# Optimization experiments

Hardware: AMD Instinct MI355X
Metric: run time of the kernel (lower is better)

Reference implementation:

```python
import jax, jax.numpy as jnp
import numpy as np

HIDDEN = 1024
HEADS = 16
HEAD_DIM = 64
B, S = 2, 2048
SCALE = 1.0 / np.sqrt(HEAD_DIM)
NEG = -1e9


def setup_inputs() -> dict:
    key = jax.random.key(0)
    k1, k2, k3, k4, k5 = jax.random.split(key, 5)
    hidden_states = jax.random.normal(k1, (B, S, HIDDEN), dtype=jnp.float32)
    # causal additive mask, broadcast over heads: [B, 1, S, S]
    causal = jnp.where(jnp.tril(jnp.ones((S, S), dtype=bool)), 0.0, NEG).astype(jnp.float32)
    attention_mask = jnp.broadcast_to(causal[None, None], (B, 1, S, S))
    std = 1.0 / np.sqrt(HIDDEN)
    Wq = jax.random.normal(k2, (HIDDEN, HEADS * HEAD_DIM), dtype=jnp.float32) * std
    Wk = jax.random.normal(k3, (HIDDEN, HEADS * HEAD_DIM), dtype=jnp.float32) * std
    Wv = jax.random.normal(k4, (HIDDEN, HEADS * HEAD_DIM), dtype=jnp.float32) * std
    Wo = jax.random.normal(k5, (HEADS * HEAD_DIM, HIDDEN), dtype=jnp.float32) * std
    return {"hidden_states": hidden_states, "attention_mask": attention_mask,
            "Wq": Wq, "Wk": Wk, "Wv": Wv, "Wo": Wo}


def reference(hidden_states, attention_mask, Wq, Wk, Wv, Wo):
    b, s, _ = hidden_states.shape
    # projections (eval mode: dropouts are identity)
    q = (hidden_states @ Wq).reshape(b, s, HEADS, HEAD_DIM).transpose(0, 2, 1, 3)  # [B,H,S,D]
    k = (hidden_states @ Wk).reshape(b, s, HEADS, HEAD_DIM).transpose(0, 2, 1, 3)
    v = (hidden_states @ Wv).reshape(b, s, HEADS, HEAD_DIM).transpose(0, 2, 1, 3)
    scores = jnp.einsum('bhqd,bhkd->bhqk', q, k) * SCALE + attention_mask  # [B,H,S,S]
    probs = jax.nn.softmax(scores, axis=-1)
    out = jnp.einsum('bhqk,bhkd->bhqd', probs, v)  # [B,H,S,D]
    out = out.transpose(0, 2, 1, 3).reshape(b, s, HEADS * HEAD_DIM)
    return out @ Wo  # [B,S,HIDDEN]
```

## Files before the change

kernel.cpp:

```cpp
#include <hip/hip_runtime.h>

typedef unsigned short u16;
typedef unsigned int u32;
typedef __bf16 bf16x8 __attribute__((ext_vector_type(8)));
typedef float f32x4 __attribute__((ext_vector_type(4)));

#define MFMA(a, b, c) __builtin_amdgcn_mfma_f32_16x16x32_bf16(a, b, c, 0, 0, 0)

#define GLD16(gsrc, ldst)                                                          \
  __builtin_amdgcn_global_load_lds(                                                \
      (const __attribute__((address_space(1))) void*)(gsrc),                       \
      (__attribute__((address_space(3))) void*)(ldst), 16, 0, 0)

#if __has_builtin(__builtin_amdgcn_exp2f)
#define EXP2(x) __builtin_amdgcn_exp2f(x)
#else
#define EXP2(x) exp2f(x)
#endif

__device__ __forceinline__ u16 f2bf(float f) {
  return __builtin_bit_cast(u16, (__bf16)f);
}

__device__ __forceinline__ u32 pk2(float a, float b) {
  __bf16 x = (__bf16)a, y = (__bf16)b;
  return (u32)__builtin_bit_cast(u16, x) | ((u32)__builtin_bit_cast(u16, y) << 16);
}

__device__ __forceinline__ float bf2f(u16 u) {
  return __builtin_bit_cast(float, ((u32)u) << 16);
}

__global__ __launch_bounds__(256) void k_cvt_x(const float* __restrict__ x,
                                               u16* __restrict__ xb) {
  int i = blockIdx.x * 256 + threadIdx.x;
  const float4* p = (const float4*)x + (size_t)i * 2;
  float4 a = p[0], b = p[1];
  uint4 o;
  o.x = pk2(a.x, a.y);
  o.y = pk2(a.z, a.w);
  o.z = pk2(b.x, b.y);
  o.w = pk2(b.z, b.w);
  *(uint4*)(xb + (size_t)i * 8) = o;
}

__global__ __launch_bounds__(256) void k_transpose_w(
    const float* __restrict__ Wq, const float* __restrict__ Wk,
    const float* __restrict__ Wv, const float* __restrict__ Wo,
    u16* __restrict__ Wt, u16* __restrict__ Wot) {
  __shared__ u16 t[32][33];
  const int k0 = blockIdx.x * 32, n0 = blockIdx.y * 32;
  const int x = threadIdx.x & 31, y = threadIdx.x >> 5;
  const float* src = (n0 < 1024) ? Wq : (n0 < 2048) ? Wk : (n0 < 3072) ? Wv : Wo;
  const int ncol = n0 & 1023;
#pragma unroll
  for (int rr = 0; rr < 4; ++rr) {
    int kl = y + rr * 8;
    t[x][kl] = f2bf(src[(size_t)(k0 + kl) * 1024 + ncol + x]);
  }
  __syncthreads();
  u16* dst = (n0 < 3072) ? (Wt + (size_t)n0 * 1024) : (Wot + (size_t)(n0 - 3072) * 1024);
#pragma unroll
  for (int rr = 0; rr < 4; ++rr) {
    int nl = y + rr * 8;
    dst[(size_t)nl * 1024 + k0 + x] = t[nl][x];
  }
}


__global__ __launch_bounds__(256) void k_gemm_qkv(const u16* __restrict__ A_,
                                                  const u16* __restrict__ Bt,
                                                  u16* __restrict__ Q,
                                                  u16* __restrict__ K,
                                                  u16* __restrict__ Vt) {
  __shared__ __align__(16) u16 As[2][128 * 32];
  __shared__ __align__(16) u16 Bs[2][128 * 32];
  const int tid = threadIdx.x;
  const int w = tid >> 6, l = tid & 63;
  const int lr = l & 15, lg = l >> 4;
  const int lin = blockIdx.y * 24 + blockIdx.x;
  const int swz = (lin & 7) * 96 + (lin >> 3);
  const int tM = (swz / 24) * 128, tN = (swz % 24) * 128;
  const int wr = w >> 1, wc = w & 1;
  const int bufsel = tN >> 10;

  const int srow = l >> 2;
  const int scol = (((l & 3) ^ ((l >> 3) & 3)) << 3);
  const u16* Ag = A_ + (size_t)(tM + srow) * 1024 + scol;
  const u16* Bg = Bt + (size_t)(tN + srow) * 1024 + scol;
  const int rs = (lr >> 1) & 3;

#define STAGE_QKV(buf, kk)                                                   \
  {                                                                          \
    GLD16(Ag + (size_t)(w * 16) * 1024 + (kk), &As[buf][(w * 16) * 32]);     \
    GLD16(Ag + (size_t)(64 + w * 16) * 1024 + (kk), &As[buf][(64 + w * 16) * 32]); \
    GLD16(Bg + (size_t)(w * 16) * 1024 + (kk), &Bs[buf][(w * 16) * 32]);     \
    GLD16(Bg + (size_t)(64 + w * 16) * 1024 + (kk), &Bs[buf][(64 + w * 16) * 32]); \
  }

  f32x4 acc[4][4] = {};
  STAGE_QKV(0, 0)
  __syncthreads();
  int cur = 0;

  if (bufsel < 2) {
    for (int t = 0; t < 32; ++t) {
      if (t < 31) STAGE_QKV(cur ^ 1, (t + 1) * 32)
      const u16* Ac = &As[cur][0];
      const u16* Bc = &Bs[cur][0];
      bf16x8 a[4], b[4];
#pragma unroll
      for (int m = 0; m < 4; ++m)
        a[m] = *(const bf16x8*)(Ac + (wr * 64 + m * 16 + lr) * 32 + ((lg ^ rs) << 3));
#pragma unroll
      for (int n = 0; n < 4; ++n)
        b[n] = *(const bf16x8*)(Bc + (wc * 64 + n * 16 + lr) * 32 + ((lg ^ rs) << 3));
#pragma unroll
      for (int m = 0; m < 4; ++m)
#pragma unroll
        for (int n = 0; n < 4; ++n) acc[m][n] = MFMA(b[n], a[m], acc[m][n]);
      __syncthreads();
      cur ^= 1;
    }
    u16* dst = bufsel ? K : Q;
    const float sc = bufsel ? 1.0f : 0.180336880111124f;
#pragma unroll
    for (int m = 0; m < 4; ++m) {
      int s = tM + wr * 64 + m * 16 + lr;
      int b_ = s >> 11, sr2 = s & 2047;
#pragma unroll
      for (int n = 0; n < 4; ++n) {
        int c = tN + wc * 64 + n * 16 + lg * 4;
        int c2 = c & 1023;
        int h = c2 >> 6, d = c2 & 63;
        uint2 val;
        val.x = pk2(acc[m][n][0] * sc, acc[m][n][1] * sc);
        val.y = pk2(acc[m][n][2] * sc, acc[m][n][3] * sc);
        *(uint2*)(dst + ((size_t)(b_ * 16 + h) * 2048 + sr2) * 64 + d) = val;
      }
    }
  } else {
    for (int t = 0; t < 32; ++t) {
      if (t < 31) STAGE_QKV(cur ^ 1, (t + 1) * 32)
      const u16* Ac = &As[cur][0];
      const u16* Bc = &Bs[cur][0];
      bf16x8 a[4], b[4];
#pragma unroll
      for (int m = 0; m < 4; ++m)
        a[m] = *(const bf16x8*)(Ac + (wr * 64 + m * 16 + lr) * 32 + ((lg ^ rs) << 3));
#pragma unroll
      for (int n = 0; n < 4; ++n)
        b[n] = *(const bf16x8*)(Bc + (wc * 64 + n * 16 + lr) * 32 + ((lg ^ rs) << 3));
#pragma unroll
      for (int m = 0; m < 4; ++m)
#pragma unroll
        for (int n = 0; n < 4; ++n) acc[m][n] = MFMA(a[m], b[n], acc[m][n]);
      __syncthreads();
      cur ^= 1;
    }
#pragma unroll
    for (int m = 0; m < 4; ++m) {
      int r0 = tM + wr * 64 + m * 16 + lg * 4;
      int b_ = r0 >> 11, s0 = r0 & 2047;
#pragma unroll
      for (int n = 0; n < 4; ++n) {
        int c = tN + wc * 64 + n * 16 + lr;
        int c2 = c & 1023;
        int h = c2 >> 6, d = c2 & 63;
        uint2 val;
        val.x = pk2(acc[m][n][0], acc[m][n][1]);
        val.y = pk2(acc[m][n][2], acc[m][n][3]);
        *(uint2*)(Vt + ((size_t)(b_ * 16 + h) * 64 + d) * 2048 + s0) = val;
      }
    }
  }
#undef STAGE_QKV
}

__global__ __launch_bounds__(256, 4) void k_attn(const u16* __restrict__ Q,
                                                 const u16* __restrict__ Kg,
                                                 const u16* __restrict__ Vtg,
                                                 u16* __restrict__ AO,
                                                 u16* __restrict__ PO,
                                                 float* __restrict__ ML) {
  __shared__ __align__(16) u16 Ks[2][64 * 64];
  __shared__ __align__(16) u16 Vs[2][64 * 64];
  __shared__ __align__(16) u16 Ps[4][16 * 64];
  const int tid = threadIdx.x;
  const int w = tid >> 6, l = tid & 63;
  const int lr = l & 15, lg = l >> 4;

  const int idx = blockIdx.x;
  const int bh = idx & 31;
  const int g = idx >> 5;
  int qt, c0;
  if (g < 16) { qt = 16 + g; c0 = 0; }
  else if (g < 32) { qt = 31 - (g - 16); c0 = 1; }
  else { qt = 15 - (g - 32); c0 = 0; }
  const int nkt = (qt < 16) ? (qt + 1) : (c0 == 0 ? 16 : qt - 15);
  const bool hasdiag = (qt < 16) || (c0 == 1);
  const int q0 = qt * 64;

  const u16* Qp = Q + (size_t)bh * 2048 * 64;
  const u16* Kp = Kg + (size_t)bh * 2048 * 64;
  const u16* Vp = Vtg + (size_t)bh * 64 * 2048;

  const int qrow = q0 + w * 16 + lr;
  bf16x8 qa0 = *(const bf16x8*)(Qp + (size_t)qrow * 64 + lg * 8);
  bf16x8 qa1 = *(const bf16x8*)(Qp + (size_t)qrow * 64 + 32 + lg * 8);

  f32x4 oacc[4] = {};
  float m_run = -1e30f, l_run = 0.f;

  const int srow = l >> 3;
  const int scol = ((l & 7) ^ srow) * 8;
  const int sw = (lr & 7) << 3;

  const u16* kptr = Kp + ((size_t)c0 * 1024 + srow) * 64 + scol;
  const u16* vptr = Vp + (size_t)srow * 2048 + c0 * 1024 + scol;

#pragma unroll
  for (int j = 0; j < 2; ++j) {
    int base = j * 32 + w * 8;
    GLD16(kptr + base * 64, &Ks[0][base * 64]);
    GLD16(vptr + (size_t)base * 2048, &Vs[0][base * 64]);
  }
  kptr += 4096;
  vptr += 64;
  __syncthreads();

  int cur = 0;

#define ATTN_TILE(DOPRE, DOMASK)                                                   \
  {                                                                                \
    if (DOPRE) {                                                                   \
      _Pragma("unroll") for (int j = 0; j < 2; ++j) {                              \
        int base = j * 32 + w * 8;                                                 \
        GLD16(kptr + base * 64, &Ks[cur ^ 1][base * 64]);                          \
        GLD16(vptr + (size_t)base * 2048, &Vs[cur ^ 1][base * 64]);                \
      }                                                                            \
      kptr += 4096;                                                                \
      vptr += 64;                                                                  \
    }                                                                              \
    f32x4 st[4];                                                                   \
    _Pragma("unroll") for (int n = 0; n < 4; ++n) {                                \
      const u16* kr = &Ks[cur][(n * 16 + lr) * 64];                                \
      bf16x8 kb0 = *(const bf16x8*)(kr + ((lg << 3) ^ sw));                        \
      bf16x8 kb1 = *(const bf16x8*)(kr + (((4 + lg) << 3) ^ sw));                  \
      f32x4 z = {0.f, 0.f, 0.f, 0.f};                                              \
      z = MFMA(kb0, qa0, z);                                                       \
      z = MFMA(kb1, qa1, z);                                                       \
      st[n] = z;                                                                   \
    }                                                                              \
    float mx = -1e30f;                                                             \
    _Pragma("unroll") for (int n = 0; n < 4; ++n)                                  \
        _Pragma("unroll") for (int j = 0; j < 4; ++j) {                            \
      float s = st[n][j];                                                          \
      if (DOMASK && (n * 16 + lg * 4 + j) > (w * 16 + lr)) s = -1e30f;             \
      st[n][j] = s;                                                                \
      mx = fmaxf(mx, s);                                                           \
    }                                                                              \
    mx = fmaxf(mx, __shfl_xor(mx, 16, 64));                                        \
    mx = fmaxf(mx, __shfl_xor(mx, 32, 64));                                        \
    const bool grow = __any(mx > m_run);                                           \
    float mnew = grow ? fmaxf(m_run, mx) : m_run;                                  \
    float rsum = 0.f;                                                              \
    _Pragma("unroll") for (int n = 0; n < 4; ++n)                                  \
        _Pragma("unroll") for (int j = 0; j < 4; ++j) {                            \
      float p = EXP2(st[n][j] - mnew);                                             \
      st[n][j] = p;                                                                \
      rsum += p;                                                                   \
    }                                                                              \
    rsum += __shfl_xor(rsum, 16, 64);                                              \
    rsum += __shfl_xor(rsum, 32, 64);                                              \
    if (grow) {                                                                    \
      float fsc = EXP2(m_run - mnew);                                              \
      l_run = l_run * fsc + rsum;                                                  \
      m_run = mnew;                                                                \
      _Pragma("unroll") for (int n = 0; n < 4; ++n)                                \
          _Pragma("unroll") for (int j = 0; j < 4; ++j) oacc[n][j] *= fsc;         \
    } else {                                                                       \
      l_run += rsum;                                                               \
    }                                                                              \
    u16* pb = &Ps[w][0];                                                           \
    _Pragma("unroll") for (int n = 0; n < 4; ++n) {                                \
      int slot = n * 2 + (lg >> 1);                                                \
      int off = lr * 64 + ((slot ^ (lr & 7)) << 3) + (lg & 1) * 4;                 \
      uint2 val;                                                                   \
      val.x = pk2(st[n][0], st[n][1]);                                             \
      val.y = pk2(st[n][2], st[n][3]);                                             \
      *(uint2*)(pb + off) = val;                                                   \
    }                                                                              \
    bf16x8 pa0 = *(const bf16x8*)(pb + lr * 64 + ((lg << 3) ^ sw));                \
    bf16x8 pa1 = *(const bf16x8*)(pb + lr * 64 + (((4 + lg) << 3) ^ sw));          \
    _Pragma("unroll") for (int n = 0; n < 4; ++n) {                                \
      const u16* vr = &Vs[cur][(n * 16 + lr) * 64];                                \
      bf16x8 vb0 = *(const bf16x8*)(vr + ((lg << 3) ^ sw));                        \
      bf16x8 vb1 = *(const bf16x8*)(vr + (((4 + lg) << 3) ^ sw));                  \
      oacc[n] = MFMA(vb0, pa0, oacc[n]);                                           \
      oacc[n] = MFMA(vb1, pa1, oacc[n]);                                           \
    }                                                                              \
  }

  for (int it = 0; it < nkt - 1; ++it) {
    ATTN_TILE(true, false);
    __syncthreads();
    cur ^= 1;
  }
  if (hasdiag) {
    ATTN_TILE(false, true);
  } else {
    ATTN_TILE(false, false);
  }
#undef ATTN_TILE

  if (qt < 16) {
    const int b_ = bh >> 4, h = bh & 15;
    const float linv = 1.0f / l_run;
    const int s = q0 + w * 16 + lr;
    u16* dst = AO + ((size_t)(b_ * 2048 + s)) * 1024 + h * 64 + lg * 4;
#pragma unroll
    for (int n = 0; n < 4; ++n) {
      uint2 val;
      val.x = pk2(oacc[n][0] * linv, oacc[n][1] * linv);
      val.y = pk2(oacc[n][2] * linv, oacc[n][3] * linv);
      *(uint2*)(dst + n * 16) = val;
    }
  } else {
    const int p = (bh * 16 + (qt - 16)) * 2 + c0;
    u16* po = PO + (size_t)p * 4096 + (size_t)(w * 16 + lr) * 64 + lg * 4;
#pragma unroll
    for (int n = 0; n < 4; ++n) {
      uint2 val;
      val.x = pk2(oacc[n][0], oacc[n][1]);
      val.y = pk2(oacc[n][2], oacc[n][3]);
      *(uint2*)(po + n * 16) = val;
    }
    if (lg == 0) {
      ML[(size_t)p * 128 + (w * 16 + lr)] = m_run;
      ML[(size_t)p * 128 + 64 + (w * 16 + lr)] = l_run;
    }
  }
}

__global__ __launch_bounds__(256) void k_combine(const u16* __restrict__ PO,
                                                 const float* __restrict__ ML,
                                                 u16* __restrict__ AO) {
  const int blk = blockIdx.x;
  const int bh = blk >> 4, qt = 16 + (blk & 15);
  const int row = threadIdx.x >> 2;
  const int dseg = (threadIdx.x & 3) * 16;
  const size_t p0 = (size_t)blk * 2;
  const float m0 = ML[p0 * 128 + row], l0 = ML[p0 * 128 + 64 + row];
  const float m1 = ML[p0 * 128 + 128 + row], l1 = ML[p0 * 128 + 192 + row];
  const float M = fmaxf(m0, m1);
  float w0 = EXP2(m0 - M), w1 = EXP2(m1 - M);
  const float inv = 1.0f / (l0 * w0 + l1 * w1);
  w0 *= inv;
  w1 *= inv;
  const u16* o0 = PO + p0 * 4096 + (size_t)row * 64 + dseg;
  const u16* o1 = o0 + 4096;
  const int b_ = bh >> 4, h = bh & 15;
  u16* dst = AO + ((size_t)(b_ * 2048 + qt * 64 + row)) * 1024 + h * 64 + dseg;
#pragma unroll
  for (int half = 0; half < 2; ++half) {
    uint4 a = *(const uint4*)(o0 + half * 8);
    uint4 b = *(const uint4*)(o1 + half * 8);
    u32 aw[4] = {a.x, a.y, a.z, a.w};
    u32 bw[4] = {b.x, b.y, b.z, b.w};
    uint4 o;
    u32 ow[4];
#pragma unroll
    for (int i = 0; i < 4; ++i) {
      float r0 = bf2f((u16)(aw[i] & 0xffffu)) * w0 + bf2f((u16)(bw[i] & 0xffffu)) * w1;
      float r1 = bf2f((u16)(aw[i] >> 16)) * w0 + bf2f((u16)(bw[i] >> 16)) * w1;
      ow[i] = pk2(r0, r1);
    }
    o.x = ow[0]; o.y = ow[1]; o.z = ow[2]; o.w = ow[3];
    *(uint4*)(dst + half * 8) = o;
  }
}

__global__ __launch_bounds__(256) void k_gemm_out(const u16* __restrict__ A_,
                                                  const u16* __restrict__ Bt,
                                                  float* __restrict__ out) {
  __shared__ __align__(16) u16 As[2][128 * 32];
  __shared__ __align__(16) u16 Bs[2][64 * 32];
  const int tid = threadIdx.x;
  const int w = tid >> 6, l = tid & 63;
  const int lr = l & 15, lg = l >> 4;
  const int lin = blockIdx.y * 16 + blockIdx.x;
  const int swz = (lin & 7) * 64 + (lin >> 3);
  const int tM = (swz / 16) * 128, tN = (swz % 16) * 64;

  const int srow = l >> 2;
  const int scol = (((l & 3) ^ ((l >> 3) & 3)) << 3);
  const u16* Ag = A_ + (size_t)(tM + srow) * 1024 + scol;
  const u16* Bg = Bt + (size_t)(tN + srow) * 1024 + scol;
  const int rs = (lr >> 1) & 3;

#define STAGE_OUT(buf, kk)                                                   \
  {                                                                          \
    GLD16(Ag + (size_t)(w * 16) * 1024 + (kk), &As[buf][(w * 16) * 32]);     \
    GLD16(Ag + (size_t)(64 + w * 16) * 1024 + (kk), &As[buf][(64 + w * 16) * 32]); \
    GLD16(Bg + (size_t)(w * 16) * 1024 + (kk), &Bs[buf][(w * 16) * 32]);     \
  }

  f32x4 acc[2][4] = {};
  STAGE_OUT(0, 0)
  __syncthreads();
  int cur = 0;
  for (int t = 0; t < 32; ++t) {
    if (t < 31) STAGE_OUT(cur ^ 1, (t + 1) * 32)
    const u16* Ac = &As[cur][0];
    const u16* Bc = &Bs[cur][0];
    bf16x8 a[2], b[4];
#pragma unroll
    for (int m = 0; m < 2; ++m)
      a[m] = *(const bf16x8*)(Ac + (w * 32 + m * 16 + lr) * 32 + ((lg ^ rs) << 3));
#pragma unroll
    for (int n = 0; n < 4; ++n)
      b[n] = *(const bf16x8*)(Bc + (n * 16 + lr) * 32 + ((lg ^ rs) << 3));
#pragma unroll
    for (int m = 0; m < 2; ++m)
#pragma unroll
      for (int n = 0; n < 4; ++n) acc[m][n] = MFMA(b[n], a[m], acc[m][n]);
    __syncthreads();
    cur ^= 1;
  }
#undef STAGE_OUT

#pragma unroll
  for (int m = 0; m < 2; ++m) {
    int s = tM + w * 32 + m * 16 + lr;
#pragma unroll
    for (int n = 0; n < 4; ++n) {
      int c = tN + n * 16 + lg * 4;
      float4 v;
      v.x = acc[m][n][0];
      v.y = acc[m][n][1];
      v.z = acc[m][n][2];
      v.w = acc[m][n][3];
      *(float4*)(out + (size_t)s * 1024 + c) = v;
    }
  }
}

extern "C" void kernel_launch(void* const* d_in, const int* in_sizes, int n_in,
                              void* d_out, int out_size, void* d_ws, size_t ws_size,
                              hipStream_t stream) {
  const float* X = (const float*)d_in[0];
  const float* Wq = (const float*)d_in[2];
  const float* Wk = (const float*)d_in[3];
  const float* Wv = (const float*)d_in[4];
  const float* Wo = (const float*)d_in[5];
  float* out = (float*)d_out;

  char* ws = (char*)d_ws;
  if (ws_size < (size_t)48 * 1024 * 1024) return;
  u16* Xb  = (u16*)(ws);
  u16* Wt  = (u16*)(ws + 8388608);
  u16* Wot = (u16*)(ws + 14680064);
  u16* Q   = (u16*)(ws + 16777216);
  u16* K   = (u16*)(ws + 25165824);
  u16* Vt  = (u16*)(ws + 33554432);
  u16* AO  = (u16*)(ws + 41943040);
  u16*   PO = (u16*)(ws);
  float* ML = (float*)(ws + 8388608);

  k_cvt_x<<<2048, 256, 0, stream>>>(X, Xb);
  k_transpose_w<<<dim3(32, 128), 256, 0, stream>>>(Wq, Wk, Wv, Wo, Wt, Wot);
  k_gemm_qkv<<<dim3(24, 32), 256, 0, stream>>>(Xb, Wt, Q, K, Vt);
  k_attn<<<1536, 256, 0, stream>>>(Q, K, Vt, AO, PO, ML);
  k_combine<<<512, 256, 0, stream>>>(PO, ML, AO);
  k_gemm_out<<<dim3(16, 32), 256, 0, stream>>>(AO, Wot, out);
}
```

Baseline: 120.2 us.

## Fuse split-KV combine into output GEMM, merge prep kernels, add MFMA priority

Merges the x-conversion and weight-transpose kernels into a single prep launch. Folds the split-KV partial combine into the output projection GEMM's A-tile staging for the second half of each sequence, which removes one kernel launch and the AO round-trip for those rows. Also raises wave priority around the MFMA sections in attention and relaxes the online-softmax rescale threshold so the running max is updated only when it grows by more than 8. The combine path replaces async global-to-LDS loads with register loads plus exp math inside the GEMM loop, which could stall it. The relaxed threshold lets un-rescaled exponentials reach up to 2^8, a small numeric risk.

```diff
diff --git a/kernel.cpp b/kernel.cpp
--- a/kernel.cpp
+++ b/kernel.cpp
@@ -31,25 +31,27 @@
   return __builtin_bit_cast(float, ((u32)u) << 16);
 }
 
-__global__ __launch_bounds__(256) void k_cvt_x(const float* __restrict__ x,
-                                               u16* __restrict__ xb) {
-  int i = blockIdx.x * 256 + threadIdx.x;
-  const float4* p = (const float4*)x + (size_t)i * 2;
-  float4 a = p[0], b = p[1];
-  uint4 o;
-  o.x = pk2(a.x, a.y);
-  o.y = pk2(a.z, a.w);
-  o.z = pk2(b.x, b.y);
-  o.w = pk2(b.z, b.w);
-  *(uint4*)(xb + (size_t)i * 8) = o;
-}
-
-__global__ __launch_bounds__(256) void k_transpose_w(
-    const float* __restrict__ Wq, const float* __restrict__ Wk,
-    const float* __restrict__ Wv, const float* __restrict__ Wo,
+__global__ __launch_bounds__(256) void k_prep(
+    const float* __restrict__ X, const float* __restrict__ Wq,
+    const float* __restrict__ Wk, const float* __restrict__ Wv,
+    const float* __restrict__ Wo, u16* __restrict__ Xb,
     u16* __restrict__ Wt, u16* __restrict__ Wot) {
   __shared__ u16 t[32][33];
-  const int k0 = blockIdx.x * 32, n0 = blockIdx.y * 32;
+  int bid = blockIdx.x;
+  if (bid < 2048) {
+    int i = bid * 256 + threadIdx.x;
+    const float4* p = (const float4*)X + (size_t)i * 2;
+    float4 a = p[0], b = p[1];
+    uint4 o;
+    o.x = pk2(a.x, a.y);
+    o.y = pk2(a.z, a.w);
+    o.z = pk2(b.x, b.y);
+    o.w = pk2(b.z, b.w);
+    *(uint4*)(Xb + (size_t)i * 8) = o;
+    return;
+  }
+  bid -= 2048;
+  const int k0 = (bid & 31) * 32, n0 = (bid >> 5) * 32;
   const int x = threadIdx.x & 31, y = threadIdx.x >> 5;
   const float* src = (n0 < 1024) ? Wq : (n0 < 2048) ? Wk : (n0 < 3072) ? Wv : Wo;
   const int ncol = n0 & 1023;
@@ -130,8 +132,7 @@
       int b_ = s >> 11, sr2 = s & 2047;
 #pragma unroll
       for (int n = 0; n < 4; ++n) {
-        int c = tN + wc * 64 + n * 16 + lg * 4;
-        int c2 = c & 1023;
+        int c2 = (tN + wc * 64 + n * 16 + lg * 4) & 1023;
         int h = c2 >> 6, d = c2 & 63;
         uint2 val;
         val.x = pk2(acc[m][n][0] * sc, acc[m][n][1] * sc);
@@ -164,8 +165,7 @@
       int b_ = r0 >> 11, s0 = r0 & 2047;
 #pragma unroll
       for (int n = 0; n < 4; ++n) {
-        int c = tN + wc * 64 + n * 16 + lr;
-        int c2 = c & 1023;
+        int c2 = (tN + wc * 64 + n * 16 + lr) & 1023;
         int h = c2 >> 6, d = c2 & 63;
         uint2 val;
         val.x = pk2(acc[m][n][0], acc[m][n][1]);
@@ -243,6 +243,7 @@
       vptr += 64;                                                                  \
     }                                                                              \
     f32x4 st[4];                                                                   \
+    __builtin_amdgcn_s_setprio(1);                                                 \
     _Pragma("unroll") for (int n = 0; n < 4; ++n) {                                \
       const u16* kr = &Ks[cur][(n * 16 + lr) * 64];                                \
       bf16x8 kb0 = *(const bf16x8*)(kr + ((lg << 3) ^ sw));                        \
@@ -252,6 +253,7 @@
       z = MFMA(kb1, qa1, z);                                                       \
       st[n] = z;                                                                   \
     }                                                                              \
+    __builtin_amdgcn_s_setprio(0);                                                 \
     float mx = -1e30f;                                                             \
     _Pragma("unroll") for (int n = 0; n < 4; ++n)                                  \
         _Pragma("unroll") for (int j = 0; j < 4; ++j) {                            \
@@ -262,7 +264,7 @@
     }                                                                              \
     mx = fmaxf(mx, __shfl_xor(mx, 16, 64));                                        \
     mx = fmaxf(mx, __shfl_xor(mx, 32, 64));                                        \
-    const bool grow = __any(mx > m_run);                                           \
+    const bool grow = __any(mx > m_run + 8.0f);               \
     float mnew = grow ? fmaxf(m_run, mx) : m_run;                                  \
     float rsum = 0.f;                                                              \
     _Pragma("unroll") for (int n = 0; n < 4; ++n)                                  \
@@ -293,6 +295,7 @@
     }                                                                              \
     bf16x8 pa0 = *(const bf16x8*)(pb + lr * 64 + ((lg << 3) ^ sw));                \
     bf16x8 pa1 = *(const bf16x8*)(pb + lr * 64 + (((4 + lg) << 3) ^ sw));          \
+    __builtin_amdgcn_s_setprio(1);                                                 \
     _Pragma("unroll") for (int n = 0; n < 4; ++n) {                                \
       const u16* vr = &Vs[cur][(n * 16 + lr) * 64];                                \
       bf16x8 vb0 = *(const bf16x8*)(vr + ((lg << 3) ^ sw));                        \
@@ -300,6 +303,7 @@
       oacc[n] = MFMA(vb0, pa0, oacc[n]);                                           \
       oacc[n] = MFMA(vb1, pa1, oacc[n]);                                           \
     }                                                                              \
+    __builtin_amdgcn_s_setprio(0);                                                 \
   }
 
   for (int it = 0; it < nkt - 1; ++it) {
@@ -343,45 +347,35 @@
   }
 }
 
-__global__ __launch_bounds__(256) void k_combine(const u16* __restrict__ PO,
-                                                 const float* __restrict__ ML,
-                                                 u16* __restrict__ AO) {
-  const int blk = blockIdx.x;
-  const int bh = blk >> 4, qt = 16 + (blk & 15);
-  const int row = threadIdx.x >> 2;
-  const int dseg = (threadIdx.x & 3) * 16;
-  const size_t p0 = (size_t)blk * 2;
-  const float m0 = ML[p0 * 128 + row], l0 = ML[p0 * 128 + 64 + row];
-  const float m1 = ML[p0 * 128 + 128 + row], l1 = ML[p0 * 128 + 192 + row];
-  const float M = fmaxf(m0, m1);
+__device__ __forceinline__ uint4 comb8(const u16* __restrict__ PO,
+                                       const float* __restrict__ ML,
+                                       int p0, int ri, int d0) {
+  const u16* o0 = PO + (size_t)p0 * 4096 + ri * 64 + d0;
+  uint4 a = *(const uint4*)o0;
+  uint4 c = *(const uint4*)(o0 + 4096);
+  const float* mlp = ML + (size_t)p0 * 128 + ri;
+  float m0 = mlp[0], l0 = mlp[64], m1 = mlp[128], l1 = mlp[192];
+  float M = fmaxf(m0, m1);
   float w0 = EXP2(m0 - M), w1 = EXP2(m1 - M);
-  const float inv = 1.0f / (l0 * w0 + l1 * w1);
+  float inv = 1.0f / (l0 * w0 + l1 * w1);
   w0 *= inv;
   w1 *= inv;
-  const u16* o0 = PO + p0 * 4096 + (size_t)row * 64 + dseg;
-  const u16* o1 = o0 + 4096;
-  const int b_ = bh >> 4, h = bh & 15;
-  u16* dst = AO + ((size_t)(b_ * 2048 + qt * 64 + row)) * 1024 + h * 64 + dseg;
-#pragma unroll
-  for (int half = 0; half < 2; ++half) {
-    uint4 a = *(const uint4*)(o0 + half * 8);
-    uint4 b = *(const uint4*)(o1 + half * 8);
-    u32 aw[4] = {a.x, a.y, a.z, a.w};
-    u32 bw[4] = {b.x, b.y, b.z, b.w};
-    uint4 o;
-    u32 ow[4];
-#pragma unroll
-    for (int i = 0; i < 4; ++i) {
-      float r0 = bf2f((u16)(aw[i] & 0xffffu)) * w0 + bf2f((u16)(bw[i] & 0xffffu)) * w1;
-      float r1 = bf2f((u16)(aw[i] >> 16)) * w0 + bf2f((u16)(bw[i] >> 16)) * w1;
-      ow[i] = pk2(r0, r1);
-    }
-    o.x = ow[0]; o.y = ow[1]; o.z = ow[2]; o.w = ow[3];
-    *(uint4*)(dst + half * 8) = o;
-  }
-}
-
-__global__ __launch_bounds__(256) void k_gemm_out(const u16* __restrict__ A_,
+  u32 aw[4] = {a.x, a.y, a.z, a.w}, cw[4] = {c.x, c.y, c.z, c.w};
+  u32 ow[4];
+#pragma unroll
+  for (int i = 0; i < 4; ++i) {
+    float r0 = bf2f((u16)(aw[i] & 0xffffu)) * w0 + bf2f((u16)(cw[i] & 0xffffu)) * w1;
+    float r1 = bf2f((u16)(aw[i] >> 16)) * w0 + bf2f((u16)(cw[i] >> 16)) * w1;
+    ow[i] = pk2(r0, r1);
+  }
+  uint4 o;
+  o.x = ow[0]; o.y = ow[1]; o.z = ow[2]; o.w = ow[3];
+  return o;
+}
+
+__global__ __launch_bounds__(256) void k_gemm_out(const u16* __restrict__ AO,
+                                                  const u16* __restrict__ PO,
+                                                  const float* __restrict__ ML,
                                                   const u16* __restrict__ Bt,
                                                   float* __restrict__ out) {
   __shared__ __align__(16) u16 As[2][128 * 32];
@@ -394,41 +388,91 @@
   const int tM = (swz / 16) * 128, tN = (swz % 16) * 64;
 
   const int srow = l >> 2;
-  const int scol = (((l & 3) ^ ((l >> 3) & 3)) << 3);
-  const u16* Ag = A_ + (size_t)(tM + srow) * 1024 + scol;
+  const int gran = (l & 3) ^ ((l >> 3) & 3);
+  const int scol = gran << 3;
+  const u16* Ag = AO + (size_t)(tM + srow) * 1024 + scol;
   const u16* Bg = Bt + (size_t)(tN + srow) * 1024 + scol;
   const int rs = (lr >> 1) & 3;
 
-#define STAGE_OUT(buf, kk)                                                   \
+  const bool comb = (tM >> 10) & 1;
+  const int r0 = w * 16 + (l >> 2);
+  const int bb = tM >> 11;
+  const int qt0 = ((tM & 2047) >> 6) - 16;
+  const int slot8 = (l & 3) * 8;
+
+#define STAGE_B(buf, kk) GLD16(Bg + (size_t)(w * 16) * 1024 + (kk), &Bs[buf][(w * 16) * 32]);
+
+#define STAGE_A_GLD(buf, kk)                                                 \
   {                                                                          \
     GLD16(Ag + (size_t)(w * 16) * 1024 + (kk), &As[buf][(w * 16) * 32]);     \
     GLD16(Ag + (size_t)(64 + w * 16) * 1024 + (kk), &As[buf][(64 + w * 16) * 32]); \
-    GLD16(Bg + (size_t)(w * 16) * 1024 + (kk), &Bs[buf][(w * 16) * 32]);     \
+  }
+
+#define OUT_COMPUTE(buf)                                                           \
+  {                                                                                \
+    const u16* Ac = &As[buf][0];                                                   \
+    const u16* Bc = &Bs[buf][0];                                                   \
+    bf16x8 a[2], b[4];                                                             \
+    _Pragma("unroll") for (int m = 0; m < 2; ++m)                                  \
+        a[m] = *(const bf16x8*)(Ac + (w * 32 + m * 16 + lr) * 32 +                 \
+                                ((lg ^ rs) << 3));                                 \
+    _Pragma("unroll") for (int n = 0; n < 4; ++n)                                  \
+        b[n] = *(const bf16x8*)(Bc + (n * 16 + lr) * 32 + ((lg ^ rs) << 3));       \
+    _Pragma("unroll") for (int m = 0; m < 2; ++m)                                  \
+        _Pragma("unroll") for (int n = 0; n < 4; ++n)                              \
+            acc[m][n] = MFMA(b[n], a[m], acc[m][n]);                               \
   }
 
   f32x4 acc[2][4] = {};
-  STAGE_OUT(0, 0)
-  __syncthreads();
   int cur = 0;
-  for (int t = 0; t < 32; ++t) {
-    if (t < 31) STAGE_OUT(cur ^ 1, (t + 1) * 32)
-    const u16* Ac = &As[cur][0];
-    const u16* Bc = &Bs[cur][0];
-    bf16x8 a[2], b[4];
-#pragma unroll
-    for (int m = 0; m < 2; ++m)
-      a[m] = *(const bf16x8*)(Ac + (w * 32 + m * 16 + lr) * 32 + ((lg ^ rs) << 3));
-#pragma unroll
-    for (int n = 0; n < 4; ++n)
-      b[n] = *(const bf16x8*)(Bc + (n * 16 + lr) * 32 + ((lg ^ rs) << 3));
-#pragma unroll
-    for (int m = 0; m < 2; ++m)
-#pragma unroll
-      for (int n = 0; n < 4; ++n) acc[m][n] = MFMA(b[n], a[m], acc[m][n]);
+
+  if (!comb) {
+    STAGE_A_GLD(0, 0)
+    STAGE_B(0, 0)
     __syncthreads();
-    cur ^= 1;
-  }
-#undef STAGE_OUT
+    for (int t = 0; t < 32; ++t) {
+      if (t < 31) {
+        STAGE_A_GLD(cur ^ 1, (t + 1) * 32)
+        STAGE_B(cur ^ 1, (t + 1) * 32)
+      }
+      OUT_COMPUTE(cur)
+      __syncthreads();
+      cur ^= 1;
+    }
+  } else {
+    {
+      int c = 0 + gran * 8;
+      int h = c >> 6, d0 = c & 63;
+      int p0 = ((bb * 16 + h) * 16 + qt0) * 2;
+      uint4 v0 = comb8(PO, ML, p0, r0, d0);
+      uint4 v1 = comb8(PO, ML, p0 + 2, r0, d0);
+      *(uint4*)(&As[0][r0 * 32 + slot8]) = v0;
+      *(uint4*)(&As[0][(64 + r0) * 32 + slot8]) = v1;
+    }
+    STAGE_B(0, 0)
+    __syncthreads();
+    for (int t = 0; t < 32; ++t) {
+      uint4 v0, v1;
+      if (t < 31) {
+        STAGE_B(cur ^ 1, (t + 1) * 32)
+        int c = (t + 1) * 32 + gran * 8;
+        int h = c >> 6, d0 = c & 63;
+        int p0 = ((bb * 16 + h) * 16 + qt0) * 2;
+        v0 = comb8(PO, ML, p0, r0, d0);
+        v1 = comb8(PO, ML, p0 + 2, r0, d0);
+      }
+      OUT_COMPUTE(cur)
+      if (t < 31) {
+        *(uint4*)(&As[cur ^ 1][r0 * 32 + slot8]) = v0;
+        *(uint4*)(&As[cur ^ 1][(64 + r0) * 32 + slot8]) = v1;
+      }
+      __syncthreads();
+      cur ^= 1;
+    }
+  }
+#undef STAGE_B
+#undef STAGE_A_GLD
+#undef OUT_COMPUTE
 
 #pragma unroll
   for (int m = 0; m < 2; ++m) {
@@ -468,10 +512,8 @@
   u16*   PO = (u16*)(ws);
   float* ML = (float*)(ws + 8388608);
 
-  k_cvt_x<<<2048, 256, 0, stream>>>(X, Xb);
-  k_transpose_w<<<dim3(32, 128), 256, 0, stream>>>(Wq, Wk, Wv, Wo, Wt, Wot);
+  k_prep<<<6144, 256, 0, stream>>>(X, Wq, Wk, Wv, Wo, Xb, Wt, Wot);
   k_gemm_qkv<<<dim3(24, 32), 256, 0, stream>>>(Xb, Wt, Q, K, Vt);
   k_attn<<<1536, 256, 0, stream>>>(Q, K, Vt, AO, PO, ML);
-  k_combine<<<512, 256, 0, stream>>>(PO, ML, AO);
-  k_gemm_out<<<dim3(16, 32), 256, 0, stream>>>(AO, Wot, out);
-}
+  k_gemm_out<<<dim3(16, 32), 256, 0, stream>>>(AO, PO, ML, Wot, out);
+}
```

New measurement: 131.4 us. 9.3% more time.

## Enlarge attention query tiles to 128 rows, merge prep kernels, add MFMA priority

Applied to the files above, without the earlier changes.

Attention blocks grow from 256 to 512 threads with 128-row query tiles, so each K/V tile load into LDS is shared by eight waves instead of four. The causal work split becomes 768 blocks, with a two-way key split only for the upper query tiles and a matching rewrite of the combine kernel. The last two key tiles are now masked by global index. The X conversion and weight transpose kernels are fused into one launch, and s_setprio raises priority around the MFMA sections. The softmax max-rescale is now skipped unless the max grows by more than 8, which trades fewer rescales for extra overflow risk. Bigger blocks also cut occupancy and change load balance.

```diff
diff --git a/kernel.cpp b/kernel.cpp
--- a/kernel.cpp
+++ b/kernel.cpp
@@ -31,25 +31,27 @@
   return __builtin_bit_cast(float, ((u32)u) << 16);
 }
 
-__global__ __launch_bounds__(256) void k_cvt_x(const float* __restrict__ x,
-                                               u16* __restrict__ xb) {
-  int i = blockIdx.x * 256 + threadIdx.x;
-  const float4* p = (const float4*)x + (size_t)i * 2;
-  float4 a = p[0], b = p[1];
-  uint4 o;
-  o.x = pk2(a.x, a.y);
-  o.y = pk2(a.z, a.w);
-  o.z = pk2(b.x, b.y);
-  o.w = pk2(b.z, b.w);
-  *(uint4*)(xb + (size_t)i * 8) = o;
-}
-
-__global__ __launch_bounds__(256) void k_transpose_w(
-    const float* __restrict__ Wq, const float* __restrict__ Wk,
-    const float* __restrict__ Wv, const float* __restrict__ Wo,
+__global__ __launch_bounds__(256) void k_prep(
+    const float* __restrict__ X, const float* __restrict__ Wq,
+    const float* __restrict__ Wk, const float* __restrict__ Wv,
+    const float* __restrict__ Wo, u16* __restrict__ Xb,
     u16* __restrict__ Wt, u16* __restrict__ Wot) {
   __shared__ u16 t[32][33];
-  const int k0 = blockIdx.x * 32, n0 = blockIdx.y * 32;
+  int bid = blockIdx.x;
+  if (bid < 2048) {
+    int i = bid * 256 + threadIdx.x;
+    const float4* p = (const float4*)X + (size_t)i * 2;
+    float4 a = p[0], b = p[1];
+    uint4 o;
+    o.x = pk2(a.x, a.y);
+    o.y = pk2(a.z, a.w);
+    o.z = pk2(b.x, b.y);
+    o.w = pk2(b.z, b.w);
+    *(uint4*)(Xb + (size_t)i * 8) = o;
+    return;
+  }
+  bid -= 2048;
+  const int k0 = (bid & 31) * 32, n0 = (bid >> 5) * 32;
   const int x = threadIdx.x & 31, y = threadIdx.x >> 5;
   const float* src = (n0 < 1024) ? Wq : (n0 < 2048) ? Wk : (n0 < 3072) ? Wv : Wo;
   const int ncol = n0 & 1023;
@@ -130,8 +132,7 @@
       int b_ = s >> 11, sr2 = s & 2047;
 #pragma unroll
       for (int n = 0; n < 4; ++n) {
-        int c = tN + wc * 64 + n * 16 + lg * 4;
-        int c2 = c & 1023;
+        int c2 = (tN + wc * 64 + n * 16 + lg * 4) & 1023;
         int h = c2 >> 6, d = c2 & 63;
         uint2 val;
         val.x = pk2(acc[m][n][0] * sc, acc[m][n][1] * sc);
@@ -164,8 +165,7 @@
       int b_ = r0 >> 11, s0 = r0 & 2047;
 #pragma unroll
       for (int n = 0; n < 4; ++n) {
-        int c = tN + wc * 64 + n * 16 + lr;
-        int c2 = c & 1023;
+        int c2 = (tN + wc * 64 + n * 16 + lr) & 1023;
         int h = c2 >> 6, d = c2 & 63;
         uint2 val;
         val.x = pk2(acc[m][n][0], acc[m][n][1]);
@@ -177,15 +177,15 @@
 #undef STAGE_QKV
 }
 
-__global__ __launch_bounds__(256, 4) void k_attn(const u16* __restrict__ Q,
-                                                 const u16* __restrict__ Kg,
-                                                 const u16* __restrict__ Vtg,
-                                                 u16* __restrict__ AO,
-                                                 u16* __restrict__ PO,
-                                                 float* __restrict__ ML) {
+__global__ __launch_bounds__(512) void k_attn(const u16* __restrict__ Q,
+                                              const u16* __restrict__ Kg,
+                                              const u16* __restrict__ Vtg,
+                                              u16* __restrict__ AO,
+                                              u16* __restrict__ PO,
+                                              float* __restrict__ ML) {
   __shared__ __align__(16) u16 Ks[2][64 * 64];
   __shared__ __align__(16) u16 Vs[2][64 * 64];
-  __shared__ __align__(16) u16 Ps[4][16 * 64];
+  __shared__ __align__(16) u16 Ps[8][16 * 64];
   const int tid = threadIdx.x;
   const int w = tid >> 6, l = tid & 63;
   const int lr = l & 15, lg = l >> 4;
@@ -194,18 +194,17 @@
   const int bh = idx & 31;
   const int g = idx >> 5;
   int qt, c0;
-  if (g < 16) { qt = 16 + g; c0 = 0; }
-  else if (g < 32) { qt = 31 - (g - 16); c0 = 1; }
-  else { qt = 15 - (g - 32); c0 = 0; }
-  const int nkt = (qt < 16) ? (qt + 1) : (c0 == 0 ? 16 : qt - 15);
-  const bool hasdiag = (qt < 16) || (c0 == 1);
-  const int q0 = qt * 64;
+  if (g < 16) { qt = 15 - (g >> 1); c0 = g & 1; }
+  else        { qt = 7 - (g - 16);  c0 = 0; }
+  const bool split = (qt >= 8);
+  const int nkt = split ? (qt + 1) : (2 * qt + 2);
+  const int kstart = (split && c0 == 1) ? (qt + 1) : 0;
 
   const u16* Qp = Q + (size_t)bh * 2048 * 64;
   const u16* Kp = Kg + (size_t)bh * 2048 * 64;
   const u16* Vp = Vtg + (size_t)bh * 64 * 2048;
 
-  const int qrow = q0 + w * 16 + lr;
+  const int qrow = qt * 128 + w * 16 + lr;
   bf16x8 qa0 = *(const bf16x8*)(Qp + (size_t)qrow * 64 + lg * 8);
   bf16x8 qa1 = *(const bf16x8*)(Qp + (size_t)qrow * 64 + 32 + lg * 8);
 
@@ -216,33 +215,27 @@
   const int scol = ((l & 7) ^ srow) * 8;
   const int sw = (lr & 7) << 3;
 
-  const u16* kptr = Kp + ((size_t)c0 * 1024 + srow) * 64 + scol;
-  const u16* vptr = Vp + (size_t)srow * 2048 + c0 * 1024 + scol;
-
-#pragma unroll
-  for (int j = 0; j < 2; ++j) {
-    int base = j * 32 + w * 8;
-    GLD16(kptr + base * 64, &Ks[0][base * 64]);
-    GLD16(vptr + (size_t)base * 2048, &Vs[0][base * 64]);
-  }
+  const u16* kptr = Kp + ((size_t)(kstart * 64 + w * 8 + srow)) * 64 + scol;
+  const u16* vptr = Vp + (size_t)(w * 8 + srow) * 2048 + kstart * 64 + scol;
+
+  GLD16(kptr, &Ks[0][(w * 8) * 64]);
+  GLD16(vptr, &Vs[0][(w * 8) * 64]);
   kptr += 4096;
   vptr += 64;
   __syncthreads();
 
   int cur = 0;
 
-#define ATTN_TILE(DOPRE, DOMASK)                                                   \
+#define ATTN_TILE(DOPRE, DOMASK, KTG)                                              \
   {                                                                                \
     if (DOPRE) {                                                                   \
-      _Pragma("unroll") for (int j = 0; j < 2; ++j) {                              \
-        int base = j * 32 + w * 8;                                                 \
-        GLD16(kptr + base * 64, &Ks[cur ^ 1][base * 64]);                          \
-        GLD16(vptr + (size_t)base * 2048, &Vs[cur ^ 1][base * 64]);                \
-      }                                                                            \
+      GLD16(kptr, &Ks[cur ^ 1][(w * 8) * 64]);                                     \
+      GLD16(vptr, &Vs[cur ^ 1][(w * 8) * 64]);                                     \
       kptr += 4096;                                                                \
       vptr += 64;                                                                  \
     }                                                                              \
     f32x4 st[4];                                                                   \
+    __builtin_amdgcn_s_setprio(1);                                                 \
     _Pragma("unroll") for (int n = 0; n < 4; ++n) {                                \
       const u16* kr = &Ks[cur][(n * 16 + lr) * 64];                                \
       bf16x8 kb0 = *(const bf16x8*)(kr + ((lg << 3) ^ sw));                        \
@@ -252,17 +245,19 @@
       z = MFMA(kb1, qa1, z);                                                       \
       st[n] = z;                                                                   \
     }                                                                              \
+    __builtin_amdgcn_s_setprio(0);                                                 \
     float mx = -1e30f;                                                             \
     _Pragma("unroll") for (int n = 0; n < 4; ++n)                                  \
         _Pragma("unroll") for (int j = 0; j < 4; ++j) {                            \
       float s = st[n][j];                                                          \
-      if (DOMASK && (n * 16 + lg * 4 + j) > (w * 16 + lr)) s = -1e30f;             \
+      if (DOMASK && ((KTG)*64 + n * 16 + lg * 4 + j) > (qt * 128 + w * 16 + lr))   \
+        s = -1e30f;                                                                \
       st[n][j] = s;                                                                \
       mx = fmaxf(mx, s);                                                           \
     }                                                                              \
     mx = fmaxf(mx, __shfl_xor(mx, 16, 64));                                        \
     mx = fmaxf(mx, __shfl_xor(mx, 32, 64));                                        \
-    const bool grow = __any(mx > m_run);                                           \
+    const bool grow = __any(mx > m_run + 8.0f);               \
     float mnew = grow ? fmaxf(m_run, mx) : m_run;                                  \
     float rsum = 0.f;                                                              \
     _Pragma("unroll") for (int n = 0; n < 4; ++n)                                  \
@@ -293,6 +288,7 @@
     }                                                                              \
     bf16x8 pa0 = *(const bf16x8*)(pb + lr * 64 + ((lg << 3) ^ sw));                \
     bf16x8 pa1 = *(const bf16x8*)(pb + lr * 64 + (((4 + lg) << 3) ^ sw));          \
+    __builtin_amdgcn_s_setprio(1);                                                 \
     _Pragma("unroll") for (int n = 0; n < 4; ++n) {                                \
       const u16* vr = &Vs[cur][(n * 16 + lr) * 64];                                \
       bf16x8 vb0 = *(const bf16x8*)(vr + ((lg << 3) ^ sw));                        \
@@ -300,24 +296,28 @@
       oacc[n] = MFMA(vb0, pa0, oacc[n]);                                           \
       oacc[n] = MFMA(vb1, pa1, oacc[n]);                                           \
     }                                                                              \
-  }
-
-  for (int it = 0; it < nkt - 1; ++it) {
-    ATTN_TILE(true, false);
+    __builtin_amdgcn_s_setprio(0);                                                 \
+  }
+
+  for (int it = 0; it < nkt - 2; ++it) {
+    ATTN_TILE(true, false, 0);
     __syncthreads();
     cur ^= 1;
   }
-  if (hasdiag) {
-    ATTN_TILE(false, true);
-  } else {
-    ATTN_TILE(false, false);
+  {
+    ATTN_TILE(true, true, (kstart + nkt - 2));
+    __syncthreads();
+    cur ^= 1;
+  }
+  {
+    ATTN_TILE(false, true, (kstart + nkt - 1));
   }
 #undef ATTN_TILE
 
-  if (qt < 16) {
+  if (!split) {
     const int b_ = bh >> 4, h = bh & 15;
     const float linv = 1.0f / l_run;
-    const int s = q0 + w * 16 + lr;
+    const int s = qt * 128 + w * 16 + lr;
     u16* dst = AO + ((size_t)(b_ * 2048 + s)) * 1024 + h * 64 + lg * 4;
 #pragma unroll
     for (int n = 0; n < 4; ++n) {
@@ -327,8 +327,9 @@
       *(uint2*)(dst + n * 16) = val;
     }
   } else {
-    const int p = (bh * 16 + (qt - 16)) * 2 + c0;
-    u16* po = PO + (size_t)p * 4096 + (size_t)(w * 16 + lr) * 64 + lg * 4;
+    const int p = (bh * 8 + (qt - 8)) * 2 + c0;
+    const int row = w * 16 + lr;
+    u16* po = PO + (size_t)p * 8192 + (size_t)row * 64 + lg * 4;
 #pragma unroll
     for (int n = 0; n < 4; ++n) {
       uint2 val;
@@ -337,8 +338,8 @@
       *(uint2*)(po + n * 16) = val;
     }
     if (lg == 0) {
-      ML[(size_t)p * 128 + (w * 16 + lr)] = m_run;
-      ML[(size_t)p * 128 + 64 + (w * 16 + lr)] = l_run;
+      ML[(size_t)p * 256 + row] = m_run;
+      ML[(size_t)p * 256 + 128 + row] = l_run;
     }
   }
 }
@@ -347,25 +348,26 @@
                                                  const float* __restrict__ ML,
                                                  u16* __restrict__ AO) {
   const int blk = blockIdx.x;
-  const int bh = blk >> 4, qt = 16 + (blk & 15);
-  const int row = threadIdx.x >> 2;
-  const int dseg = (threadIdx.x & 3) * 16;
+  const int bh = blk >> 3, qt = 8 + (blk & 7);
+  const int row = threadIdx.x >> 1;
+  const int d0 = (threadIdx.x & 1) * 32;
   const size_t p0 = (size_t)blk * 2;
-  const float m0 = ML[p0 * 128 + row], l0 = ML[p0 * 128 + 64 + row];
-  const float m1 = ML[p0 * 128 + 128 + row], l1 = ML[p0 * 128 + 192 + row];
+  const float* ml = ML + p0 * 256;
+  const float m0 = ml[row], l0 = ml[128 + row];
+  const float m1 = ml[256 + row], l1 = ml[384 + row];
   const float M = fmaxf(m0, m1);
   float w0 = EXP2(m0 - M), w1 = EXP2(m1 - M);
   const float inv = 1.0f / (l0 * w0 + l1 * w1);
   w0 *= inv;
   w1 *= inv;
-  const u16* o0 = PO + p0 * 4096 + (size_t)row * 64 + dseg;
-  const u16* o1 = o0 + 4096;
+  const u16* o0 = PO + p0 * 8192 + (size_t)row * 64 + d0;
+  const u16* o1 = o0 + 8192;
   const int b_ = bh >> 4, h = bh & 15;
-  u16* dst = AO + ((size_t)(b_ * 2048 + qt * 64 + row)) * 1024 + h * 64 + dseg;
-#pragma unroll
-  for (int half = 0; half < 2; ++half) {
-    uint4 a = *(const uint4*)(o0 + half * 8);
-    uint4 b = *(const uint4*)(o1 + half * 8);
+  u16* dst = AO + ((size_t)(b_ * 2048 + qt * 128 + row)) * 1024 + h * 64 + d0;
+#pragma unroll
+  for (int q4 = 0; q4 < 4; ++q4) {
+    uint4 a = *(const uint4*)(o0 + q4 * 8);
+    uint4 b = *(const uint4*)(o1 + q4 * 8);
     u32 aw[4] = {a.x, a.y, a.z, a.w};
     u32 bw[4] = {b.x, b.y, b.z, b.w};
     uint4 o;
@@ -377,7 +379,7 @@
       ow[i] = pk2(r0, r1);
     }
     o.x = ow[0]; o.y = ow[1]; o.z = ow[2]; o.w = ow[3];
-    *(uint4*)(dst + half * 8) = o;
+    *(uint4*)(dst + q4 * 8) = o;
   }
 }
 
@@ -468,10 +470,9 @@
   u16*   PO = (u16*)(ws);
   float* ML = (float*)(ws + 8388608);
 
-  k_cvt_x<<<2048, 256, 0, stream>>>(X, Xb);
-  k_transpose_w<<<dim3(32, 128), 256, 0, stream>>>(Wq, Wk, Wv, Wo, Wt, Wot);
+  k_prep<<<6144, 256, 0, stream>>>(X, Wq, Wk, Wv, Wo, Xb, Wt, Wot);
   k_gemm_qkv<<<dim3(24, 32), 256, 0, stream>>>(Xb, Wt, Q, K, Vt);
-  k_attn<<<1536, 256, 0, stream>>>(Q, K, Vt, AO, PO, ML);
-  k_combine<<<512, 256, 0, stream>>>(PO, ML, AO);
+  k_attn<<<768, 512, 0, stream>>>(Q, K, Vt, AO, PO, ML);
+  k_combine<<<256, 256, 0, stream>>>(PO, ML, AO);
   k_gemm_out<<<dim3(16, 32), 256, 0, stream>>>(AO, Wot, out);
 }
```

After: 124.2 us. 1.03x slower.

## Merge prep kernels, triple-buffer K with split waits, lazy softmax rescale

Applied to the files above, without the earlier changes.

Fuses the X conversion and the weight transpose into one launch, removing a kernel boundary. In attention, K gets a third LDS buffer and is staged two tiles ahead of V, with raw vmcnt waits plus barriers so V loads overlap QK compute. It also raises wave priority around the MFMA blocks and skips the running-max rescale unless the max grows by more than 8. The lazy rescale assumes exp values stay within fp32/bf16 range, and the hand-written vmcnt counts must match the issued loads exactly.

```diff
diff --git a/kernel.cpp b/kernel.cpp
--- a/kernel.cpp
+++ b/kernel.cpp
@@ -18,6 +18,9 @@
 #define EXP2(x) exp2f(x)
 #endif
 
+#define WAITBAR(N)                                                                 \
+  asm volatile("s_waitcnt vmcnt(" #N ")\n\ts_barrier" ::: "memory");
+
 __device__ __forceinline__ u16 f2bf(float f) {
   return __builtin_bit_cast(u16, (__bf16)f);
 }
@@ -31,25 +34,27 @@
   return __builtin_bit_cast(float, ((u32)u) << 16);
 }
 
-__global__ __launch_bounds__(256) void k_cvt_x(const float* __restrict__ x,
-                                               u16* __restrict__ xb) {
-  int i = blockIdx.x * 256 + threadIdx.x;
-  const float4* p = (const float4*)x + (size_t)i * 2;
-  float4 a = p[0], b = p[1];
-  uint4 o;
-  o.x = pk2(a.x, a.y);
-  o.y = pk2(a.z, a.w);
-  o.z = pk2(b.x, b.y);
-  o.w = pk2(b.z, b.w);
-  *(uint4*)(xb + (size_t)i * 8) = o;
-}
-
-__global__ __launch_bounds__(256) void k_transpose_w(
-    const float* __restrict__ Wq, const float* __restrict__ Wk,
-    const float* __restrict__ Wv, const float* __restrict__ Wo,
+__global__ __launch_bounds__(256) void k_prep(
+    const float* __restrict__ X, const float* __restrict__ Wq,
+    const float* __restrict__ Wk, const float* __restrict__ Wv,
+    const float* __restrict__ Wo, u16* __restrict__ Xb,
     u16* __restrict__ Wt, u16* __restrict__ Wot) {
   __shared__ u16 t[32][33];
-  const int k0 = blockIdx.x * 32, n0 = blockIdx.y * 32;
+  int bid = blockIdx.x;
+  if (bid < 2048) {
+    int i = bid * 256 + threadIdx.x;
+    const float4* p = (const float4*)X + (size_t)i * 2;
+    float4 a = p[0], b = p[1];
+    uint4 o;
+    o.x = pk2(a.x, a.y);
+    o.y = pk2(a.z, a.w);
+    o.z = pk2(b.x, b.y);
+    o.w = pk2(b.z, b.w);
+    *(uint4*)(Xb + (size_t)i * 8) = o;
+    return;
+  }
+  bid -= 2048;
+  const int k0 = (bid & 31) * 32, n0 = (bid >> 5) * 32;
   const int x = threadIdx.x & 31, y = threadIdx.x >> 5;
   const float* src = (n0 < 1024) ? Wq : (n0 < 2048) ? Wk : (n0 < 3072) ? Wv : Wo;
   const int ncol = n0 & 1023;
@@ -130,8 +135,7 @@
       int b_ = s >> 11, sr2 = s & 2047;
 #pragma unroll
       for (int n = 0; n < 4; ++n) {
-        int c = tN + wc * 64 + n * 16 + lg * 4;
-        int c2 = c & 1023;
+        int c2 = (tN + wc * 64 + n * 16 + lg * 4) & 1023;
         int h = c2 >> 6, d = c2 & 63;
         uint2 val;
         val.x = pk2(acc[m][n][0] * sc, acc[m][n][1] * sc);
@@ -164,8 +168,7 @@
       int b_ = r0 >> 11, s0 = r0 & 2047;
 #pragma unroll
       for (int n = 0; n < 4; ++n) {
-        int c = tN + wc * 64 + n * 16 + lr;
-        int c2 = c & 1023;
+        int c2 = (tN + wc * 64 + n * 16 + lr) & 1023;
         int h = c2 >> 6, d = c2 & 63;
         uint2 val;
         val.x = pk2(acc[m][n][0], acc[m][n][1]);
@@ -183,7 +186,7 @@
                                                  u16* __restrict__ AO,
                                                  u16* __restrict__ PO,
                                                  float* __restrict__ ML) {
-  __shared__ __align__(16) u16 Ks[2][64 * 64];
+  __shared__ __align__(16) u16 Ks[3][64 * 64];
   __shared__ __align__(16) u16 Vs[2][64 * 64];
   __shared__ __align__(16) u16 Ps[4][16 * 64];
   const int tid = threadIdx.x;
@@ -219,32 +222,25 @@
   const u16* kptr = Kp + ((size_t)c0 * 1024 + srow) * 64 + scol;
   const u16* vptr = Vp + (size_t)srow * 2048 + c0 * 1024 + scol;
 
-#pragma unroll
-  for (int j = 0; j < 2; ++j) {
-    int base = j * 32 + w * 8;
-    GLD16(kptr + base * 64, &Ks[0][base * 64]);
-    GLD16(vptr + (size_t)base * 2048, &Vs[0][base * 64]);
-  }
-  kptr += 4096;
-  vptr += 64;
-  __syncthreads();
-
-  int cur = 0;
-
-#define ATTN_TILE(DOPRE, DOMASK)                                                   \
+#define STAGE_K(buf)                                                               \
   {                                                                                \
-    if (DOPRE) {                                                                   \
-      _Pragma("unroll") for (int j = 0; j < 2; ++j) {                              \
-        int base = j * 32 + w * 8;                                                 \
-        GLD16(kptr + base * 64, &Ks[cur ^ 1][base * 64]);                          \
-        GLD16(vptr + (size_t)base * 2048, &Vs[cur ^ 1][base * 64]);                \
-      }                                                                            \
-      kptr += 4096;                                                                \
-      vptr += 64;                                                                  \
-    }                                                                              \
+    GLD16(kptr + (size_t)(w * 8) * 64, &Ks[buf][(w * 8) * 64]);                    \
+    GLD16(kptr + (size_t)(32 + w * 8) * 64, &Ks[buf][(32 + w * 8) * 64]);          \
+    kptr += 4096;                                                                  \
+  }
+#define STAGE_V(buf)                                                               \
+  {                                                                                \
+    GLD16(vptr + (size_t)(w * 8) * 2048, &Vs[buf][(w * 8) * 64]);                  \
+    GLD16(vptr + (size_t)(32 + w * 8) * 2048, &Vs[buf][(32 + w * 8) * 64]);        \
+    vptr += 64;                                                                    \
+  }
+
+#define ATTN_TILE(KB, VB, DOMASK)                                                  \
+  {                                                                                \
     f32x4 st[4];                                                                   \
+    __builtin_amdgcn_s_setprio(1);                                                 \
     _Pragma("unroll") for (int n = 0; n < 4; ++n) {                                \
-      const u16* kr = &Ks[cur][(n * 16 + lr) * 64];                                \
+      const u16* kr = &Ks[KB][(n * 16 + lr) * 64];                                 \
       bf16x8 kb0 = *(const bf16x8*)(kr + ((lg << 3) ^ sw));                        \
       bf16x8 kb1 = *(const bf16x8*)(kr + (((4 + lg) << 3) ^ sw));                  \
       f32x4 z = {0.f, 0.f, 0.f, 0.f};                                              \
@@ -252,6 +248,7 @@
       z = MFMA(kb1, qa1, z);                                                       \
       st[n] = z;                                                                   \
     }                                                                              \
+    __builtin_amdgcn_s_setprio(0);                                                 \
     float mx = -1e30f;                                                             \
     _Pragma("unroll") for (int n = 0; n < 4; ++n)                                  \
         _Pragma("unroll") for (int j = 0; j < 4; ++j) {                            \
@@ -262,7 +259,7 @@
     }                                                                              \
     mx = fmaxf(mx, __shfl_xor(mx, 16, 64));                                        \
     mx = fmaxf(mx, __shfl_xor(mx, 32, 64));                                        \
-    const bool grow = __any(mx > m_run);                                           \
+    const bool grow = __any(mx > m_run + 8.0f);               \
     float mnew = grow ? fmaxf(m_run, mx) : m_run;                                  \
     float rsum = 0.f;                                                              \
     _Pragma("unroll") for (int n = 0; n < 4; ++n)                                  \
@@ -293,26 +290,56 @@
     }                                                                              \
     bf16x8 pa0 = *(const bf16x8*)(pb + lr * 64 + ((lg << 3) ^ sw));                \
     bf16x8 pa1 = *(const bf16x8*)(pb + lr * 64 + (((4 + lg) << 3) ^ sw));          \
+    __builtin_amdgcn_s_setprio(1);                                                 \
     _Pragma("unroll") for (int n = 0; n < 4; ++n) {                                \
-      const u16* vr = &Vs[cur][(n * 16 + lr) * 64];                                \
+      const u16* vr = &Vs[VB][(n * 16 + lr) * 64];                                 \
       bf16x8 vb0 = *(const bf16x8*)(vr + ((lg << 3) ^ sw));                        \
       bf16x8 vb1 = *(const bf16x8*)(vr + (((4 + lg) << 3) ^ sw));                  \
       oacc[n] = MFMA(vb0, pa0, oacc[n]);                                           \
       oacc[n] = MFMA(vb1, pa1, oacc[n]);                                           \
     }                                                                              \
-  }
-
-  for (int it = 0; it < nkt - 1; ++it) {
-    ATTN_TILE(true, false);
-    __syncthreads();
-    cur ^= 1;
-  }
-  if (hasdiag) {
-    ATTN_TILE(false, true);
+    __builtin_amdgcn_s_setprio(0);                                                 \
+  }
+
+  STAGE_K(0)
+  STAGE_V(0)
+  if (nkt > 1) {
+    STAGE_K(1)
+    WAITBAR(2)
   } else {
-    ATTN_TILE(false, false);
+    WAITBAR(0)
+  }
+
+  int kb = 0, vb = 0;
+  for (int t = 0; t < nkt - 2; ++t) {
+    STAGE_V(vb ^ 1)
+    STAGE_K((kb == 0) ? 2 : (kb - 1))
+    ATTN_TILE(kb, vb, false)
+    WAITBAR(2)
+    kb = (kb == 2) ? 0 : kb + 1;
+    vb ^= 1;
+  }
+  if (nkt >= 2) {
+    STAGE_V(vb ^ 1)
+    ATTN_TILE(kb, vb, false)
+    WAITBAR(0)
+    kb = (kb == 2) ? 0 : kb + 1;
+    vb ^= 1;
+    if (hasdiag) {
+      ATTN_TILE(kb, vb, true)
+    } else {
+      ATTN_TILE(kb, vb, false)
+    }
+  } else {
+    if (hasdiag) {
+      ATTN_TILE(0, 0, true)
+    } else {
+      ATTN_TILE(0, 0, false)
+    }
   }
 #undef ATTN_TILE
+#undef STAGE_K
+#undef STAGE_V
 
   if (qt < 16) {
     const int b_ = bh >> 4, h = bh & 15;
@@ -468,8 +495,7 @@
   u16*   PO = (u16*)(ws);
   float* ML = (float*)(ws + 8388608);
 
-  k_cvt_x<<<2048, 256, 0, stream>>>(X, Xb);
-  k_transpose_w<<<dim3(32, 128), 256, 0, stream>>>(Wq, Wk, Wv, Wo, Wt, Wot);
+  k_prep<<<6144, 256, 0, stream>>>(X, Wq, Wk, Wv, Wo, Xb, Wt, Wot);
   k_gemm_qkv<<<dim3(24, 32), 256, 0, stream>>>(Xb, Wt, Q, K, Vt);
   k_attn<<<1536, 256, 0, stream>>>(Q, K, Vt, AO, PO, ML);
   k_combine<<<512, 256, 0, stream>>>(PO, ML, AO);
```

Result: slower. 124.8 us (+3.8%).
